# Kernel optimization log

Measured on AMD Instinct MI355X. Metric: run time of the kernel, lower is better.

Reference implementation:

```python
import jax, jax.numpy as jnp
import numpy as np

K = 3          # kernel size
STRIDE = 1
# padding=0, dilation=1, groups=1 (torchvision DeformConv2d defaults for args not passed)


def _offset_conv(x, w_off, b_off):
    # plain VALID conv, NCHW / OIHW
    out = jax.lax.conv_general_dilated(
        x, w_off, window_strides=(STRIDE, STRIDE), padding='VALID',
        dimension_numbers=('NCHW', 'OIHW', 'NCHW'))
    return out + b_off[None, :, None, None]


def _bilinear_sample(xp, ys, xs):
    # xp: [B,H,W,C]; ys/xs: [B,KK,Ho,Wo] fractional sample coords
    B, H, W, _ = xp.shape
    y0f = jnp.floor(ys)
    x0f = jnp.floor(xs)
    wy = ys - y0f
    wx = xs - x0f
    y0 = y0f.astype(jnp.int32)
    x0 = x0f.astype(jnp.int32)
    b = jnp.arange(B)[:, None, None, None]

    def gather(yi, xi):
        valid = (yi >= 0) & (yi < H) & (xi >= 0) & (xi < W)
        yc = jnp.clip(yi, 0, H - 1)
        xc = jnp.clip(xi, 0, W - 1)
        return xp[b, yc, xc] * valid[..., None].astype(xp.dtype)

    v00 = gather(y0, x0)
    v01 = gather(y0, x0 + 1)
    v10 = gather(y0 + 1, x0)
    v11 = gather(y0 + 1, x0 + 1)
    w00 = ((1 - wy) * (1 - wx))[..., None]
    w01 = ((1 - wy) * wx)[..., None]
    w10 = (wy * (1 - wx))[..., None]
    w11 = (wy * wx)[..., None]
    return v00 * w00 + v01 * w01 + v10 * w10 + v11 * w11  # [B,KK,Ho,Wo,C]


def _mdconv_block(x, w_off, b_off, weight, bias):
    B, Cin, H, W = x.shape
    KK = K * K
    off_out = _offset_conv(x, w_off, b_off)            # [B, 3*KK, Ho, Wo]
    Ho, Wo = off_out.shape[2], off_out.shape[3]
    o1 = off_out[:, :KK]
    o2 = off_out[:, KK:2 * KK]
    mask = jax.nn.sigmoid(off_out[:, 2 * KK:])          # [B,KK,Ho,Wo]
    # torchvision offset layout: pairs (y, x) per kernel point, built as cat(o1, o2)
    off = jnp.concatenate([o1, o2], axis=1).reshape(B, KK, 2, Ho, Wo)
    off_y, off_x = off[:, :, 0], off[:, :, 1]

    kh = jnp.arange(KK) // K
    kw = jnp.arange(KK) % K
    base_y = jnp.arange(Ho)[None, :] * STRIDE + kh[:, None]   # [KK,Ho]
    base_x = jnp.arange(Wo)[None, :] * STRIDE + kw[:, None]   # [KK,Wo]
    ys = base_y[None, :, :, None].astype(x.dtype) + off_y     # [B,KK,Ho,Wo]
    xs = base_x[None, :, None, :].astype(x.dtype) + off_x

    xp = jnp.transpose(x, (0, 2, 3, 1))                        # [B,H,W,Cin]
    sampled = _bilinear_sample(xp, ys, xs)                     # [B,KK,Ho,Wo,Cin]
    sampled = sampled * mask[..., None]                        # modulation
    w = weight.reshape(weight.shape[0], weight.shape[1], KK)   # [Cout,Cin,KK]
    out = jnp.einsum('bkhwc,ock->bohw', sampled, w)
    out = out + bias[None, :, None, None]
    return jax.nn.relu(out)  # block's activate_func=relu; norm/pool are None


def setup_inputs() -> dict:
    key = jax.random.key(0)
    k1, k2, k3, k4, k5 = jax.random.split(key, 5)
    B, Cin, Cout, H, W = 4, 64, 64, 128, 128
    x = jax.random.normal(k1, (B, Cin, H, W), dtype=jnp.float32)
    # offset/mask conv params (original zero-inits; use small random to exercise sampling)
    w_off = jax.random.normal(k2, (3 * K * K, Cin, K, K), dtype=jnp.float32) * 0.1 / np.sqrt(Cin * K * K)
    b_off = jax.random.normal(k3, (3 * K * K,), dtype=jnp.float32) * 0.1
    fan_in = Cin * K * K
    weight = jax.random.uniform(k4, (Cout, Cin, K, K), dtype=jnp.float32,
                                minval=-1.0, maxval=1.0) / np.sqrt(fan_in)
    bias = jax.random.uniform(k5, (Cout,), dtype=jnp.float32,
                              minval=-1.0, maxval=1.0) / np.sqrt(fan_in)
    return {'x': x, 'w_off': w_off, 'b_off': b_off, 'weight': weight, 'bias': bias}


def reference(x, w_off, b_off, weight, bias):
    return _mdconv_block(x, w_off, b_off, weight, bias)
```

## Files before the change

### kernel.cpp

```cpp
#include <hip/hip_runtime.h>
#include <hip/hip_bf16.h>
#include <math.h>

namespace {
constexpr int Bn = 4, Cin = 64, Cout = 64, Hh = 128, Ww = 128, Ho = 126, Wo = 126;
constexpr int HW = Hh * Ww;
constexpr int WOB = 63;
constexpr int NBLK = Bn * Ho * 2;
constexpr int ROWU = 68;
constexpr int RSTR = 6 * 68;
}

typedef __attribute__((ext_vector_type(8))) short bf16x8;
typedef __attribute__((ext_vector_type(4))) float f32x4;

__device__ __forceinline__ unsigned short f2bf(float f) {
    __hip_bfloat16 h = __float2bfloat16(f);
    return __builtin_bit_cast(unsigned short, h);
}
__device__ __forceinline__ float bf2f(unsigned short u) {
    unsigned int v = (unsigned int)u << 16;
    return __builtin_bit_cast(float, v);
}
__device__ __forceinline__ unsigned int f2bf_pk(float lo, float hi) {
    return (unsigned int)f2bf(lo) | ((unsigned int)f2bf(hi) << 16);
}
__device__ __forceinline__ bf16x8 mk8(unsigned int u0, unsigned int u1,
                                      unsigned int u2, unsigned int u3) {
    union { unsigned int u[4]; bf16x8 v; } x;
    x.u[0] = u0; x.u[1] = u1; x.u[2] = u2; x.u[3] = u3;
    return x.v;
}
__device__ __forceinline__ int swz_block(int orig, int nwg) {
    int q = nwg >> 3, r = nwg & 7;
    int xcd = orig & 7, idx = orig >> 3;
    return (xcd < r ? xcd * (q + 1) : r * (q + 1) + (xcd - r) * q) + idx;
}

__global__ __launch_bounds__(256) void prep_transpose_kernel(
    const float* __restrict__ x, const float* __restrict__ w_off,
    const float* __restrict__ weight, unsigned int* __restrict__ xT16,
    unsigned short* __restrict__ wA_hi, unsigned short* __restrict__ wA_lo,
    unsigned short* __restrict__ wOff_hi, unsigned short* __restrict__ wOff_lo)
{
    int blk = blockIdx.x;
    if (blk < 1024) {
        __shared__ float t[64][65];
        int b    = blk >> 8;
        int hw0  = (blk & 255) * 64;
        int lane = (int)(threadIdx.x & 63);
        int w4   = (int)(threadIdx.x >> 6);

        const float* xb = x + b * (Cin * HW) + hw0;
#pragma unroll
        for (int i = 0; i < 16; ++i) {
            int cin = w4 * 16 + i;
            t[cin][lane] = xb[cin * HW + lane];
        }
        __syncthreads();
        unsigned int* dst = xT16 + ((size_t)b * HW + hw0) * 32;
        int px = (int)(threadIdx.x >> 2);
        int c8 = (int)(threadIdx.x & 3) * 8;
#pragma unroll
        for (int i = 0; i < 8; ++i) {
            int cp = c8 + i;
            dst[px * 32 + cp] = f2bf_pk(t[2 * cp][px], t[2 * cp + 1][px]);
        }
    } else {
        int i = (blk - 1024) * 256 + (int)threadIdx.x;
        if (i < 36864) {
            int j = i % 8;  int t = i / 8;
            int l = t % 64; t /= 64;
            int h = t % 2;  t /= 2;
            int w = t % 4;  int k = t / 4;
            int cout = 16 * w + (l & 15);
            int cin  = 32 * h + 8 * (l >> 4) + j;
            float v = weight[cout * 576 + cin * 9 + k];
            unsigned short hi = f2bf(v);
            wA_hi[i] = hi;
            wA_lo[i] = f2bf(v - bf2f(hi));

            int o = cout;
            float vo = o < 27 ? w_off[o * 576 + cin * 9 + k] : 0.f;
            unsigned short oh = f2bf(vo);
            wOff_hi[i] = oh;
            wOff_lo[i] = f2bf(vo - bf2f(oh));
        }
    }
}

__global__ __launch_bounds__(256, 2) void mdcn_kernel(
    const unsigned int* __restrict__ xT16, const float* __restrict__ b_off,
    const unsigned short* __restrict__ wOff_hi,
    const unsigned short* __restrict__ wOff_lo,
    const unsigned short* __restrict__ wA_hi,
    const unsigned short* __restrict__ wA_lo,
    const float* __restrict__ bias, float* __restrict__ out)
{
    __shared__ unsigned int region[32 * RSTR];
    __shared__ unsigned int lds[2][32 * ROWU];
    __shared__ float Ap[27][64];

    int wg   = swz_block(blockIdx.x, NBLK);
    int wid  = __builtin_amdgcn_readfirstlane((int)(threadIdx.x >> 6));
    int lane = (int)(threadIdx.x & 63);
    int b    = wg / 252;
    int rem  = wg - b * 252;
    int ho   = rem >> 1;
    int c0   = (rem & 1) * WOB;
    int x_lo = c0 - 1;
    int pxs  = min(lane, 62);
    int wo   = c0 + pxs;

    const unsigned int* xTb = xT16 + (size_t)b * HW * 32;

    for (int i = 0; i < 13; ++i) {
        int idx4 = (int)threadIdx.x + 256 * i;
        if (idx4 < 3264) {
            int cp4 = (idx4 & 7) * 4;
            int rc  = idx4 >> 3;
            int row = rc / 68;
            int col = rc - row * 68;
            int y = min(max(ho - 1 + row, 0), Hh - 1);
            int x = min(max(x_lo + col, 0), Ww - 1);
            uint4 q = *reinterpret_cast<const uint4*>(xTb + (y * Ww + x) * 32 + cp4);
            region[(cp4 + 0) * RSTR + rc] = q.x;
            region[(cp4 + 1) * RSTR + rc] = q.y;
            region[(cp4 + 2) * RSTR + rc] = q.z;
            region[(cp4 + 3) * RSTR + rc] = q.w;
        }
    }
    __syncthreads();

    {
        unsigned int u[8];
        auto LOADT = [&](int k) {
            int kh = k / 3, kw = k - 3 * kh;
            int off = (kh + 1) * 68 + (pxs + 1 + kw);
#pragma unroll
            for (int j = 0; j < 8; ++j)
                u[j] = region[(wid * 8 + j) * RSTR + off];
        };
        auto WRITE0 = [&](int buf) {
            unsigned int* dst = &lds[buf][(8 * wid) * ROWU + lane];
#pragma unroll
            for (int j = 0; j < 8; ++j) dst[j * ROWU] = u[j];
        };

        int ct = wid & 1;
        int t0 = (wid >> 1) * 2;
        f32x4 acc0 = {0.f, 0.f, 0.f, 0.f}, acc1 = acc0;

        LOADT(0);
        WRITE0(0);
        __syncthreads();

#pragma unroll
        for (int k = 0; k < 9; ++k) {
            int cur = k & 1;
            if (k < 8) { LOADT(k + 1); WRITE0(cur ^ 1); }
            {
                const bf16x8* waH = reinterpret_cast<const bf16x8*>(
                    wOff_hi + ((k * 4 + ct) * 2) * 512 + lane * 8);
                const bf16x8* waL = reinterpret_cast<const bf16x8*>(
                    wOff_lo + ((k * 4 + ct) * 2) * 512 + lane * 8);
                bf16x8 a0h = waH[0], a1h = waH[64];
                bf16x8 a0l = waL[0], a1l = waL[64];
                const unsigned int* Lh = &lds[cur][0];
                int g4 = (lane >> 4) * 4;
#pragma unroll
                for (int tt = 0; tt < 2; ++tt) {
                    int colp = 16 * (t0 + tt) + (lane & 15);
                    bf16x8 b0 = mk8(Lh[(g4 + 0) * ROWU + colp], Lh[(g4 + 1) * ROWU + colp],
                                    Lh[(g4 + 2) * ROWU + colp], Lh[(g4 + 3) * ROWU + colp]);
                    bf16x8 b1 = mk8(Lh[(16 + g4 + 0) * ROWU + colp], Lh[(16 + g4 + 1) * ROWU + colp],
                                    Lh[(16 + g4 + 2) * ROWU + colp], Lh[(16 + g4 + 3) * ROWU + colp]);
                    f32x4& a = tt ? acc1 : acc0;
                    a = __builtin_amdgcn_mfma_f32_16x16x32_bf16(a0h, b0, a, 0, 0, 0);
                    a = __builtin_amdgcn_mfma_f32_16x16x32_bf16(a0l, b0, a, 0, 0, 0);
                    a = __builtin_amdgcn_mfma_f32_16x16x32_bf16(a1h, b1, a, 0, 0, 0);
                    a = __builtin_amdgcn_mfma_f32_16x16x32_bf16(a1l, b1, a, 0, 0, 0);
                }
            }
            __syncthreads();
        }

#pragma unroll
        for (int tt = 0; tt < 2; ++tt) {
            f32x4 a = tt ? acc1 : acc0;
            int px = 16 * (t0 + tt) + (lane & 15);
#pragma unroll
            for (int rg = 0; rg < 4; ++rg) {
                int o = 16 * ct + 4 * (lane >> 4) + rg;
                if (o < 27) Ap[o][px] = a[rg];
            }
        }
        __syncthreads();
    }

    auto SAMPLE = [&](int k, int buf) {
        float oy = Ap[2 * k][lane];
        float ox = Ap[2 * k + 1][lane];
        float mv = Ap[18 + k][lane] + b_off[18 + k];
        float ys = (float)(ho + k / 3) + oy + b_off[2 * k];
        float xs = (float)(wo + k % 3) + ox + b_off[2 * k + 1];
        float m  = 1.0f / (1.0f + expf(-mv));
        float y0f = floorf(ys), x0f = floorf(xs);
        float wy = ys - y0f, wx = xs - x0f;
        int y0 = (int)y0f, x0 = (int)x0f;
        float vy0 = (y0 >= 0  && y0 < Hh)     ? 1.f : 0.f;
        float vy1 = (y0 >= -1 && y0 < Hh - 1) ? 1.f : 0.f;
        float vx0 = (x0 >= 0  && x0 < Ww)     ? 1.f : 0.f;
        float vx1 = (x0 >= -1 && x0 < Ww - 1) ? 1.f : 0.f;
        float W00 = (1.f - wy) * (1.f - wx) * m * vy0 * vx0;
        float W01 = (1.f - wy) * wx         * m * vy0 * vx1;
        float W10 = wy         * (1.f - wx) * m * vy1 * vx0;
        float W11 = wy         * wx         * m * vy1 * vx1;

        unsigned int cu00[8], cu01[8], cu10[8], cu11[8];
        bool ok = (y0 >= ho - 1) && (y0 <= ho + 3) &&
                  (x0 >= x_lo) && (x0 <= x_lo + 66);
        if (ok) {
            int s00 = (y0 - (ho - 1)) * 68 + (x0 - x_lo);
#pragma unroll
            for (int j = 0; j < 8; ++j) {
                int basej = (wid * 8 + j) * RSTR + s00;
                cu00[j] = region[basej];
                cu01[j] = region[basej + 1];
                cu10[j] = region[basej + 68];
                cu11[j] = region[basej + 69];
            }
        } else {
            int y0c = min(max(y0, 0), Hh - 1), y1c = min(max(y0 + 1, 0), Hh - 1);
            int x0c = min(max(x0, 0), Ww - 1), x1c = min(max(x0 + 1, 0), Ww - 1);
            const unsigned int* bw = xTb + wid * 8;
            uint4 qa, qb;
            qa = *reinterpret_cast<const uint4*>(bw + (y0c * Ww + x0c) * 32);
            qb = *reinterpret_cast<const uint4*>(bw + (y0c * Ww + x0c) * 32 + 4);
            cu00[0]=qa.x; cu00[1]=qa.y; cu00[2]=qa.z; cu00[3]=qa.w;
            cu00[4]=qb.x; cu00[5]=qb.y; cu00[6]=qb.z; cu00[7]=qb.w;
            qa = *reinterpret_cast<const uint4*>(bw + (y0c * Ww + x1c) * 32);
            qb = *reinterpret_cast<const uint4*>(bw + (y0c * Ww + x1c) * 32 + 4);
            cu01[0]=qa.x; cu01[1]=qa.y; cu01[2]=qa.z; cu01[3]=qa.w;
            cu01[4]=qb.x; cu01[5]=qb.y; cu01[6]=qb.z; cu01[7]=qb.w;
            qa = *reinterpret_cast<const uint4*>(bw + (y1c * Ww + x0c) * 32);
            qb = *reinterpret_cast<const uint4*>(bw + (y1c * Ww + x0c) * 32 + 4);
            cu10[0]=qa.x; cu10[1]=qa.y; cu10[2]=qa.z; cu10[3]=qa.w;
            cu10[4]=qb.x; cu10[5]=qb.y; cu10[6]=qb.z; cu10[7]=qb.w;
            qa = *reinterpret_cast<const uint4*>(bw + (y1c * Ww + x1c) * 32);
            qb = *reinterpret_cast<const uint4*>(bw + (y1c * Ww + x1c) * 32 + 4);
            cu11[0]=qa.x; cu11[1]=qa.y; cu11[2]=qa.z; cu11[3]=qa.w;
            cu11[4]=qb.x; cu11[5]=qb.y; cu11[6]=qb.z; cu11[7]=qb.w;
        }

        unsigned int* dst = &lds[buf][(8 * wid) * ROWU + lane];
#pragma unroll
        for (int j = 0; j < 8; ++j) {
            float c00a = bf2f((unsigned short)(cu00[j] & 0xffff));
            float c00b = bf2f((unsigned short)(cu00[j] >> 16));
            float c01a = bf2f((unsigned short)(cu01[j] & 0xffff));
            float c01b = bf2f((unsigned short)(cu01[j] >> 16));
            float c10a = bf2f((unsigned short)(cu10[j] & 0xffff));
            float c10b = bf2f((unsigned short)(cu10[j] >> 16));
            float c11a = bf2f((unsigned short)(cu11[j] & 0xffff));
            float c11b = bf2f((unsigned short)(cu11[j] >> 16));
            float s0 = W00 * c00a + W01 * c01a;
            s0 = fmaf(W10, c10a, s0); s0 = fmaf(W11, c11a, s0);
            float s1 = W00 * c00b + W01 * c01b;
            s1 = fmaf(W10, c10b, s1); s1 = fmaf(W11, c11b, s1);
            dst[j * ROWU] = f2bf_pk(s0, s1);
        }
    };

    f32x4 acc[4];
#pragma unroll
    for (int t = 0; t < 4; ++t) acc[t] = {0.f, 0.f, 0.f, 0.f};

    SAMPLE(0, 0);
    __syncthreads();

#pragma unroll
    for (int k = 0; k < 9; ++k) {
        int cur = k & 1;
        if (k < 8) SAMPLE(k + 1, cur ^ 1);
        {
            const bf16x8* waH = reinterpret_cast<const bf16x8*>(
                wA_hi + ((k * 4 + wid) * 2) * 512 + lane * 8);
            const bf16x8* waL = reinterpret_cast<const bf16x8*>(
                wA_lo + ((k * 4 + wid) * 2) * 512 + lane * 8);
            bf16x8 a0h = waH[0], a1h = waH[64];
            bf16x8 a0l = waL[0], a1l = waL[64];
            const unsigned int* Lh = &lds[cur][0];
            int g4 = (lane >> 4) * 4;
#pragma unroll
            for (int t = 0; t < 4; ++t) {
                int colp = 16 * t + (lane & 15);
                bf16x8 b0 = mk8(Lh[(g4 + 0) * ROWU + colp], Lh[(g4 + 1) * ROWU + colp],
                                Lh[(g4 + 2) * ROWU + colp], Lh[(g4 + 3) * ROWU + colp]);
                bf16x8 b1 = mk8(Lh[(16 + g4 + 0) * ROWU + colp], Lh[(16 + g4 + 1) * ROWU + colp],
                                Lh[(16 + g4 + 2) * ROWU + colp], Lh[(16 + g4 + 3) * ROWU + colp]);
                acc[t] = __builtin_amdgcn_mfma_f32_16x16x32_bf16(a0h, b0, acc[t], 0, 0, 0);
                acc[t] = __builtin_amdgcn_mfma_f32_16x16x32_bf16(a0l, b0, acc[t], 0, 0, 0);
                acc[t] = __builtin_amdgcn_mfma_f32_16x16x32_bf16(a1h, b1, acc[t], 0, 0, 0);
                acc[t] = __builtin_amdgcn_mfma_f32_16x16x32_bf16(a1l, b1, acc[t], 0, 0, 0);
            }
        }
        __syncthreads();
    }

#pragma unroll
    for (int t = 0; t < 4; ++t) {
        int ps = 16 * t + (lane & 15);
        if (ps >= WOB) continue;
        int col = c0 + ps;
#pragma unroll
        for (int rg = 0; rg < 4; ++rg) {
            int cout = 16 * wid + 4 * (lane >> 4) + rg;
            float v = acc[t][rg] + bias[cout];
            out[((b * Cout + cout) * Ho + ho) * Wo + col] = fmaxf(v, 0.f);
        }
    }
}

extern "C" void kernel_launch(void* const* d_in, const int* in_sizes, int n_in,
                              void* d_out, int out_size, void* d_ws, size_t ws_size,
                              hipStream_t stream)
{
    const float* x      = (const float*)d_in[0];
    const float* w_off  = (const float*)d_in[1];
    const float* b_off  = (const float*)d_in[2];
    const float* weight = (const float*)d_in[3];
    const float* bias   = (const float*)d_in[4];

    unsigned int* xT16 = (unsigned int*)d_ws;
    unsigned short* wA_hi   = (unsigned short*)(xT16 + (size_t)Bn * HW * 32);
    unsigned short* wA_lo   = wA_hi + 36864;
    unsigned short* wOff_hi = wA_lo + 36864;
    unsigned short* wOff_lo = wOff_hi + 36864;

    prep_transpose_kernel<<<1024 + 144, 256, 0, stream>>>(
        x, w_off, weight, xT16, wA_hi, wA_lo, wOff_hi, wOff_lo);
    mdcn_kernel<<<NBLK, 256, 0, stream>>>(xT16, b_off, wOff_hi, wOff_lo,
                                          wA_hi, wA_lo, bias, (float*)d_out);
}
```

Before: 57.03 us.

## Read offset-conv MFMA operands directly from staged region, shrink halo to 5 rows

The offset-conv loop no longer copies each tap's window from the region buffer into a double-buffered lds tile. MFMA B operands are now read straight from the channel-major region, which removes nine __syncthreads and the copy traffic. The staged halo drops from 6 to 5 rows, with a row stride of 346 words, so each block issues fewer global loads and uses less LDS. The tighter fast-path bound sends more bilinear samples to the slower global-memory fallback, and the new stride may change LDS bank conflicts on the direct reads.

Measured after the change: 53.01 us. 1.08x faster.

```diff
diff --git a/kernel.cpp b/kernel.cpp
--- a/kernel.cpp
+++ b/kernel.cpp
@@ -8,7 +8,7 @@
 constexpr int WOB = 63;
 constexpr int NBLK = Bn * Ho * 2;
 constexpr int ROWU = 68;
-constexpr int RSTR = 6 * 68;
+constexpr int RSTR = 346;
 }
 
 typedef __attribute__((ext_vector_type(8))) short bf16x8;
@@ -114,9 +114,9 @@
 
     const unsigned int* xTb = xT16 + (size_t)b * HW * 32;
 
-    for (int i = 0; i < 13; ++i) {
+    for (int i = 0; i < 11; ++i) {
         int idx4 = (int)threadIdx.x + 256 * i;
-        if (idx4 < 3264) {
+        if (idx4 < 2720) {
             int cp4 = (idx4 & 7) * 4;
             int rc  = idx4 >> 3;
             int row = rc / 68;
@@ -133,56 +133,35 @@
     __syncthreads();
 
     {
-        unsigned int u[8];
-        auto LOADT = [&](int k) {
-            int kh = k / 3, kw = k - 3 * kh;
-            int off = (kh + 1) * 68 + (pxs + 1 + kw);
-#pragma unroll
-            for (int j = 0; j < 8; ++j)
-                u[j] = region[(wid * 8 + j) * RSTR + off];
-        };
-        auto WRITE0 = [&](int buf) {
-            unsigned int* dst = &lds[buf][(8 * wid) * ROWU + lane];
-#pragma unroll
-            for (int j = 0; j < 8; ++j) dst[j * ROWU] = u[j];
-        };
-
         int ct = wid & 1;
         int t0 = (wid >> 1) * 2;
         f32x4 acc0 = {0.f, 0.f, 0.f, 0.f}, acc1 = acc0;
-
-        LOADT(0);
-        WRITE0(0);
-        __syncthreads();
+        int g4 = (lane >> 4) * 4;
 
 #pragma unroll
         for (int k = 0; k < 9; ++k) {
-            int cur = k & 1;
-            if (k < 8) { LOADT(k + 1); WRITE0(cur ^ 1); }
-            {
-                const bf16x8* waH = reinterpret_cast<const bf16x8*>(
-                    wOff_hi + ((k * 4 + ct) * 2) * 512 + lane * 8);
-                const bf16x8* waL = reinterpret_cast<const bf16x8*>(
-                    wOff_lo + ((k * 4 + ct) * 2) * 512 + lane * 8);
-                bf16x8 a0h = waH[0], a1h = waH[64];
-                bf16x8 a0l = waL[0], a1l = waL[64];
-                const unsigned int* Lh = &lds[cur][0];
-                int g4 = (lane >> 4) * 4;
-#pragma unroll
-                for (int tt = 0; tt < 2; ++tt) {
-                    int colp = 16 * (t0 + tt) + (lane & 15);
-                    bf16x8 b0 = mk8(Lh[(g4 + 0) * ROWU + colp], Lh[(g4 + 1) * ROWU + colp],
-                                    Lh[(g4 + 2) * ROWU + colp], Lh[(g4 + 3) * ROWU + colp]);
-                    bf16x8 b1 = mk8(Lh[(16 + g4 + 0) * ROWU + colp], Lh[(16 + g4 + 1) * ROWU + colp],
-                                    Lh[(16 + g4 + 2) * ROWU + colp], Lh[(16 + g4 + 3) * ROWU + colp]);
-                    f32x4& a = tt ? acc1 : acc0;
-                    a = __builtin_amdgcn_mfma_f32_16x16x32_bf16(a0h, b0, a, 0, 0, 0);
-                    a = __builtin_amdgcn_mfma_f32_16x16x32_bf16(a0l, b0, a, 0, 0, 0);
-                    a = __builtin_amdgcn_mfma_f32_16x16x32_bf16(a1h, b1, a, 0, 0, 0);
-                    a = __builtin_amdgcn_mfma_f32_16x16x32_bf16(a1l, b1, a, 0, 0, 0);
-                }
+            int kh = k / 3, kw = k - 3 * kh;
+            int roff = (kh + 1) * 68 + 1 + kw;
+            const bf16x8* waH = reinterpret_cast<const bf16x8*>(
+                wOff_hi + ((k * 4 + ct) * 2) * 512 + lane * 8);
+            const bf16x8* waL = reinterpret_cast<const bf16x8*>(
+                wOff_lo + ((k * 4 + ct) * 2) * 512 + lane * 8);
+            bf16x8 a0h = waH[0], a1h = waH[64];
+            bf16x8 a0l = waL[0], a1l = waL[64];
+#pragma unroll
+            for (int tt = 0; tt < 2; ++tt) {
+                int px = 16 * (t0 + tt) + (lane & 15);
+                int ci = roff + px;
+                bf16x8 b0 = mk8(region[(g4 + 0) * RSTR + ci], region[(g4 + 1) * RSTR + ci],
+                                region[(g4 + 2) * RSTR + ci], region[(g4 + 3) * RSTR + ci]);
+                bf16x8 b1 = mk8(region[(16 + g4 + 0) * RSTR + ci], region[(16 + g4 + 1) * RSTR + ci],
+                                region[(16 + g4 + 2) * RSTR + ci], region[(16 + g4 + 3) * RSTR + ci]);
+                f32x4& a = tt ? acc1 : acc0;
+                a = __builtin_amdgcn_mfma_f32_16x16x32_bf16(a0h, b0, a, 0, 0, 0);
+                a = __builtin_amdgcn_mfma_f32_16x16x32_bf16(a0l, b0, a, 0, 0, 0);
+                a = __builtin_amdgcn_mfma_f32_16x16x32_bf16(a1h, b1, a, 0, 0, 0);
+                a = __builtin_amdgcn_mfma_f32_16x16x32_bf16(a1l, b1, a, 0, 0, 0);
             }
-            __syncthreads();
         }
 
 #pragma unroll
@@ -218,7 +197,7 @@
         float W11 = wy         * wx         * m * vy1 * vx1;
 
         unsigned int cu00[8], cu01[8], cu10[8], cu11[8];
-        bool ok = (y0 >= ho - 1) && (y0 <= ho + 3) &&
+        bool ok = (y0 >= ho - 1) && (y0 <= ho + 2) &&
                   (x0 >= x_lo) && (x0 <= x_lo + 66);
         if (ok) {
             int s00 = (y0 - (ho - 1)) * 68 + (x0 - x_lo);
```
